# Performance work log

Measured on AMD Instinct MI355X. Metric: run time of the kernel, lower is better.

## Reference

```python
import jax, jax.numpy as jnp
import numpy as np

HIDDEN = 768

def setup_inputs() -> dict:
    key = jax.random.key(0)
    ks = jax.random.split(key, 7)
    x = jax.random.normal(ks[0], (4, 4096, HIDDEN), dtype=jnp.float32)
    s = 1.0 / np.sqrt(HIDDEN)
    Wq = jax.random.uniform(ks[1], (HIDDEN, HIDDEN), minval=-s, maxval=s, dtype=jnp.float32)
    Wk = jax.random.uniform(ks[2], (HIDDEN, HIDDEN), minval=-s, maxval=s, dtype=jnp.float32)
    Wv = jax.random.uniform(ks[3], (HIDDEN, HIDDEN), minval=-s, maxval=s, dtype=jnp.float32)
    bq = jax.random.uniform(ks[4], (HIDDEN,), minval=-s, maxval=s, dtype=jnp.float32)
    bk = jax.random.uniform(ks[5], (HIDDEN,), minval=-s, maxval=s, dtype=jnp.float32)
    bv = jax.random.uniform(ks[6], (HIDDEN,), minval=-s, maxval=s, dtype=jnp.float32)
    return {"x": x, "Wq": Wq, "bq": bq, "Wk": Wk, "bk": bk, "Wv": Wv, "bv": bv}

def reference(x, Wq, bq, Wk, bk, Wv, bv):
    # q,k,v: [b, s, d]
    q = jnp.einsum('bsd,de->bse', x, Wq.T) + bq
    k = jnp.einsum('bsd,de->bse', x, Wk.T) + bk
    v = jnp.einsum('bsd,de->bse', x, Wv.T) + bv
    scale = 1.0 / jnp.sqrt(jnp.asarray(x.shape[-1], dtype=x.dtype))
    scores = jnp.einsum('bqd,bkd->bqk', q, k) * scale  # [b, s, s]
    attn = jax.nn.softmax(scores, axis=-1)
    return jnp.einsum('bqk,bkd->bqd', attn, v)
```

## Files before the change

### kernel.cpp

```cpp
#include <hip/hip_runtime.h>
#include <stdint.h>

typedef unsigned short u16;
typedef __attribute__((ext_vector_type(8))) short    bf16x8;
typedef __attribute__((ext_vector_type(4))) float    f32x4;

__device__ __forceinline__ u16 f2bf(float f) {
    unsigned u = __float_as_uint(f);
    u = (u + 0x7fffu + ((u >> 16) & 1u)) >> 16;
    return (u16)u;
}

__device__ __forceinline__ void gload16(const u16* src, u16* dst) {
    __builtin_amdgcn_global_load_lds((const __attribute__((address_space(1))) void*)src,
                                     (__attribute__((address_space(3))) void*)dst,
                                     16, 0, 0);
}

template <int IMM>
__device__ __forceinline__ bf16x8 dsr128(uint32_t addr) {
    bf16x8 r;
    asm volatile("ds_read_b128 %0, %1 offset:%2" : "=v"(r) : "v"(addr), "i"(IMM));
    return r;
}

#define LA(ARR) ((uint32_t)(uintptr_t)(__attribute__((address_space(3))) void*)&(ARR)[0])

__global__ __launch_bounds__(256) void cast_all_kernel(const float* __restrict__ x,
                                                       const float* __restrict__ w0,
                                                       const float* __restrict__ w1,
                                                       const float* __restrict__ w2,
                                                       u16* __restrict__ xb,
                                                       u16* __restrict__ wb) {
    const int b = blockIdx.x;
    if (b < 12288) {
        int i = b * 256 + threadIdx.x;
        float4 f = ((const float4*)x)[i];
        ushort4 o;
        o.x = f2bf(f.x); o.y = f2bf(f.y); o.z = f2bf(f.z); o.w = f2bf(f.w);
        ((ushort4*)xb)[i] = o;
    } else {
        const int i2 = b - 12288;
        const int w  = i2 / 576;
        const int blk = i2 - w * 576;
        const float* src = (w == 0) ? w0 : (w == 1) ? w1 : w2;
        int i = blk * 256 + threadIdx.x;
        float4 f = ((const float4*)src)[i];
        ushort4 o;
        o.x = f2bf(f.x); o.y = f2bf(f.y); o.z = f2bf(f.z); o.w = f2bf(f.w);
        ((ushort4*)wb)[(size_t)w * 147456 + i] = o;
    }
}

__global__ __launch_bounds__(256) void transpose_bf16_kernel(const u16* __restrict__ V,
                                                             u16* __restrict__ Vt,
                                                             float* __restrict__ rsum) {
    __shared__ u16 tile[32][33];
    const int t = threadIdx.x;
    if (blockIdx.x == 0 && blockIdx.z == 0) {
        int idx = blockIdx.y * 256 + t;
        if (idx < 16384) rsum[idx] = 0.f;
    }
    const size_t z = blockIdx.z;
    const u16* Vb  = V  + z * (size_t)4096 * 2304;
    u16*       Vtb = Vt + z * (size_t)768 * 4096;
    const int c0 = blockIdx.x * 32;
    const int r0 = blockIdx.y * 32;
    const int lr = t >> 3;
    const int lc = (t & 7) * 4;
    ushort4 in = *(const ushort4*)&Vb[(size_t)(r0 + lr) * 2304 + c0 + lc];
    tile[lr][lc + 0] = in.x; tile[lr][lc + 1] = in.y;
    tile[lr][lc + 2] = in.z; tile[lr][lc + 3] = in.w;
    __syncthreads();
    ushort4 o;
    o.x = tile[lc + 0][lr]; o.y = tile[lc + 1][lr];
    o.z = tile[lc + 2][lr]; o.w = tile[lc + 3][lr];
    *(ushort4*)&Vtb[(size_t)(c0 + lr) * 4096 + r0 + lc] = o;
}

template <int EPI, int WN, int NBX, int GRP, int NGRID, int NBY, int MINW>
__global__ __launch_bounds__(256, MINW) void gemm_bt_kernel(
        const u16* __restrict__ A, const u16* __restrict__ B, void* __restrict__ Cv,
        const float* __restrict__ b0, const float* __restrict__ b1, const float* __restrict__ b2,
        float* __restrict__ rs, float s2, int K,
        int lda, int ldb, int ldc, long batchA, long batchB, long batchC) {
    __shared__ __align__(16) u16 As[128 * 64];
    __shared__ __align__(16) u16 Bs[32 * WN * 64];

    constexpr int SPX = NGRID / (8 * NBX);
    const int lin = blockIdx.x;
    const int c = lin & 7, p = lin >> 3;
    const int bxi = p % GRP;
    const int rest = p / GRP;
    const int s = rest % SPX;
    const int g = rest / SPX;
    const int bx = g * GRP + bxi;
    const int strip = c * SPX + s;
    const int by = strip % NBY;
    const int bz = strip / NBY;

    const int t = threadIdx.x;
    const long z = bz;
    const u16* Ab = A + z * batchA + (long)by * 128 * lda;
    const u16* Bb = B + z * batchB + (long)bx * (32 * WN) * ldb;

    const int lane = t & 63;
    const int wave = t >> 6;
    const int wm = wave >> 1, wn = wave & 1;
    const int quad = lane >> 4;
    const int frow = lane & 15;
    const int cc0 = quad ^ (frow & 7);

    f32x4 acc[4][WN];
#pragma unroll
    for (int i = 0; i < 4; i++)
#pragma unroll
        for (int j = 0; j < WN; j++)
#pragma unroll
            for (int e = 0; e < 4; e++) acc[i][j][e] = 0.f;

    int srow[WN], scol[WN];
#pragma unroll
    for (int j = 0; j < WN; j++) {
        const int d = t + j * 256;
        srow[j] = d >> 3;
        scol[j] = ((d & 7) ^ (srow[j] & 7)) * 8;
    }

    bf16x8 ra[4], rb[WN];
#pragma unroll
    for (int j = 0; j < 4; j++)
        ra[j] = *(const bf16x8*)(Ab + (long)srow[j] * lda + scol[j]);
#pragma unroll
    for (int j = 0; j < WN; j++)
        rb[j] = *(const bf16x8*)(Bb + (long)srow[j] * ldb + scol[j]);

    for (int kt = 0; kt < K; kt += 64) {
#pragma unroll
        for (int j = 0; j < 4; j++)
            *(bf16x8*)&As[(t + j * 256) * 8] = ra[j];
#pragma unroll
        for (int j = 0; j < WN; j++)
            *(bf16x8*)&Bs[(t + j * 256) * 8] = rb[j];
        __syncthreads();

        if (kt + 64 < K) {
            const int kn = kt + 64;
#pragma unroll
            for (int j = 0; j < 4; j++)
                ra[j] = *(const bf16x8*)(Ab + (long)srow[j] * lda + kn + scol[j]);
#pragma unroll
            for (int j = 0; j < WN; j++)
                rb[j] = *(const bf16x8*)(Bb + (long)srow[j] * ldb + kn + scol[j]);
        }

#pragma unroll
        for (int kk = 0; kk < 2; kk++) {
            const int cc = (cc0 ^ (kk * 4)) * 8;
            bf16x8 bfr[WN];
#pragma unroll
            for (int j = 0; j < WN; j++)
                bfr[j] = *(const bf16x8*)&Bs[(wn * WN * 16 + j * 16 + frow) * 64 + cc];
#pragma unroll
            for (int i = 0; i < 4; i++) {
                bf16x8 af = *(const bf16x8*)&As[(wm * 64 + i * 16 + frow) * 64 + cc];
#pragma unroll
                for (int j = 0; j < WN; j++)
                    acc[i][j] = __builtin_amdgcn_mfma_f32_16x16x32_bf16(af, bfr[j], acc[i][j], 0, 0, 0);
            }
        }
        __syncthreads();
    }

    const int m_base = by * 128 + wm * 64;
    const int n_base = bx * (32 * WN) + wn * (16 * WN);

    if (EPI == 0) {
        const int seg = n_base / 768;
        const float* bp = (seg == 0) ? b0 : (seg == 1) ? b1 : b2;
        u16* C = (u16*)Cv + z * batchC;
#pragma unroll
        for (int j = 0; j < WN; j++) {
            const int col = n_base + j * 16 + frow;
            const float bb = bp[col - seg * 768];
#pragma unroll
            for (int i = 0; i < 4; i++) {
                const int row0 = m_base + i * 16 + quad * 4;
#pragma unroll
                for (int r = 0; r < 4; r++)
                    C[(long)(row0 + r) * ldc + col] = f2bf(acc[i][j][r] + bb);
            }
        }
    } else if (EPI == 1) {
        u16* C = (u16*)Cv + z * batchC;
        float rowpart[4][4];
#pragma unroll
        for (int i = 0; i < 4; i++)
#pragma unroll
            for (int r = 0; r < 4; r++) rowpart[i][r] = 0.f;
#pragma unroll
        for (int i = 0; i < 4; i++) {
            const int row0 = m_base + i * 16 + quad * 4;
#pragma unroll
            for (int j = 0; j < WN; j++) {
                const int col = n_base + j * 16 + frow;
#pragma unroll
                for (int r = 0; r < 4; r++) {
                    float e = exp2f(acc[i][j][r] * s2);
                    C[(long)(row0 + r) * ldc + col] = f2bf(e);
                    rowpart[i][r] += e;
                }
            }
        }
#pragma unroll
        for (int i = 0; i < 4; i++)
#pragma unroll
            for (int r = 0; r < 4; r++) {
                float v = rowpart[i][r];
                v += __shfl_xor(v, 1); v += __shfl_xor(v, 2);
                v += __shfl_xor(v, 4); v += __shfl_xor(v, 8);
                if (frow == 0)
                    atomicAdd(&rs[z * 4096 + m_base + i * 16 + quad * 4 + r], v);
            }
    } else {
        float* C = (float*)Cv + z * batchC;
#pragma unroll
        for (int i = 0; i < 4; i++) {
            const int row0 = m_base + i * 16 + quad * 4;
            float inv[4];
#pragma unroll
            for (int r = 0; r < 4; r++) inv[r] = 1.0f / rs[z * 4096 + row0 + r];
#pragma unroll
            for (int j = 0; j < WN; j++) {
                const int col = n_base + j * 16 + frow;
#pragma unroll
                for (int r = 0; r < 4; r++)
                    C[(long)(row0 + r) * ldc + col] = acc[i][j][r] * inv[r];
            }
        }
    }
}

template <int NBX, int NBY, int GRP, int NGRID>
__global__ __launch_bounds__(512, 4) void gemm_tp_kernel(
        const u16* __restrict__ A, const u16* __restrict__ B, u16* __restrict__ C,
        float* __restrict__ rs, float s2, int K,
        int lda, int ldb, int ldc, long batchA, long batchB, long batchC) {
    __shared__ __align__(16) u16 As0[4096];
    __shared__ __align__(16) u16 As1[4096];
    __shared__ __align__(16) u16 Bs0[8192];
    __shared__ __align__(16) u16 Bs1[8192];

    constexpr int SPX = NGRID / (8 * NBX);
    const int lin = blockIdx.x;
    const int c = lin & 7, p = lin >> 3;
    const int bxi = p % GRP;
    const int rest = p / GRP;
    const int s = rest % SPX;
    const int g = rest / SPX;
    const int bx = g * GRP + bxi;
    const int strip = c * SPX + s;
    const int by = strip % NBY;
    const int bz = strip / NBY;

    const int t = threadIdx.x;
    const int lane = t & 63;
    const int wave = t >> 6;
    const int wm = wave >> 2, wn = wave & 3;
    const int quad = lane >> 4, frow = lane & 15;

    const u16* Ab = A + (long)bz * batchA + (long)by * 128 * lda;
    const u16* Bb = B + (long)bz * batchB + (long)bx * 256 * ldb;

    const int srow = ((t >> 3) << 1) | ((t >> 2) & 1);
    const int scol = ((t & 3) ^ ((t >> 3) & 3)) * 8;

    const uint32_t rdo2 = (uint32_t)(((frow >> 1) * 64
                        + ((frow & 1) * 4 + (quad ^ ((frow >> 1) & 3))) * 8) * 2);
    const uint32_t aof2 = (uint32_t)(wm * 2048 * 2) + rdo2;
    const uint32_t bof2 = (uint32_t)(wn * 2048 * 2) + rdo2;

    f32x4 acc[4][4];
#pragma unroll
    for (int i = 0; i < 4; i++)
#pragma unroll
        for (int j = 0; j < 4; j++)
#pragma unroll
            for (int e = 0; e < 4; e++) acc[i][j][e] = 0.f;

    auto SA = [&](u16* dst, int kofs) {
        gload16(Ab + (long)srow * lda + kofs + scol, dst + wave * 512);
    };
    auto SB = [&](u16* dst, int kofs) {
        gload16(Bb + (long)srow * ldb + kofs + scol, dst + wave * 512);
        gload16(Bb + (long)(srow + 128) * ldb + kofs + scol, dst + wave * 512 + 4096);
    };

    SA(As0, 0);  SB(Bs0, 0);
    SA(As1, 32); SB(Bs1, 32);

#define MFMA16(AF, BF)                                                           \
    __builtin_amdgcn_s_setprio(1);                                               \
    _Pragma("unroll")                                                            \
    for (int i = 0; i < 4; ++i)                                                  \
        _Pragma("unroll")                                                        \
        for (int j = 0; j < 4; ++j)                                              \
            acc[i][j] = __builtin_amdgcn_mfma_f32_16x16x32_bf16(                 \
                AF[i], BF[j], acc[i][j], 0, 0, 0);                               \
    __builtin_amdgcn_s_setprio(0);

    for (int kt = 0; kt < K; kt += 64) {
        const bool pre = (kt + 64 < K);
        bf16x8 af[4], bf[4];

        asm volatile("s_waitcnt vmcnt(3)" ::: "memory");
        __builtin_amdgcn_s_barrier();
        {
            const uint32_t aAd = LA(As0) + aof2;
            const uint32_t aBd = LA(Bs0) + bof2;
            af[0] = dsr128<0>(aAd);    af[1] = dsr128<1024>(aAd);
            af[2] = dsr128<2048>(aAd); af[3] = dsr128<3072>(aAd);
            bf[0] = dsr128<0>(aBd);    bf[1] = dsr128<1024>(aBd);
            bf[2] = dsr128<2048>(aBd); bf[3] = dsr128<3072>(aBd);
        }
        asm volatile("s_waitcnt lgkmcnt(0)" ::: "memory");
        __builtin_amdgcn_sched_barrier(0);
        __builtin_amdgcn_s_barrier();
        if (pre) { SA(As0, kt + 64); SB(Bs0, kt + 64); }
        __builtin_amdgcn_sched_barrier(0);
        MFMA16(af, bf)

        if (pre) asm volatile("s_waitcnt vmcnt(3)" ::: "memory");
        else     asm volatile("s_waitcnt vmcnt(0)" ::: "memory");
        __builtin_amdgcn_s_barrier();
        {
            const uint32_t aAd = LA(As1) + aof2;
            const uint32_t aBd = LA(Bs1) + bof2;
            af[0] = dsr128<0>(aAd);    af[1] = dsr128<1024>(aAd);
            af[2] = dsr128<2048>(aAd); af[3] = dsr128<3072>(aAd);
            bf[0] = dsr128<0>(aBd);    bf[1] = dsr128<1024>(aBd);
            bf[2] = dsr128<2048>(aBd); bf[3] = dsr128<3072>(aBd);
        }
        asm volatile("s_waitcnt lgkmcnt(0)" ::: "memory");
        __builtin_amdgcn_sched_barrier(0);
        __builtin_amdgcn_s_barrier();
        if (pre) { SA(As1, kt + 96); SB(Bs1, kt + 96); }
        __builtin_amdgcn_sched_barrier(0);
        MFMA16(af, bf)
    }
#undef MFMA16

    const int m_base = by * 128 + wm * 64;
    const int n_base = bx * 256 + wn * 64;
    const long z = bz;
    u16* Cb = C + z * batchC;
#pragma unroll
    for (int i = 0; i < 4; ++i) {
        const int row0 = m_base + i * 16 + quad * 4;
        float rp[4] = {0.f, 0.f, 0.f, 0.f};
#pragma unroll
        for (int j = 0; j < 4; ++j) {
            const int col = n_base + j * 16 + frow;
#pragma unroll
            for (int r = 0; r < 4; ++r) {
                float e = exp2f(acc[i][j][r] * s2);
                Cb[(long)(row0 + r) * ldc + col] = f2bf(e);
                rp[r] += e;
            }
        }
#pragma unroll
        for (int r = 0; r < 4; ++r) {
            float v = rp[r];
            v += __shfl_xor(v, 1); v += __shfl_xor(v, 2);
            v += __shfl_xor(v, 4); v += __shfl_xor(v, 8);
            if (frow == 0) atomicAdd(&rs[z * 4096 + row0 + r], v);
        }
    }
}

extern "C" void kernel_launch(void* const* d_in, const int* in_sizes, int n_in,
                              void* d_out, int out_size, void* d_ws, size_t ws_size,
                              hipStream_t stream) {
    const float* x  = (const float*)d_in[0];
    const float* Wq = (const float*)d_in[1];
    const float* bq = (const float*)d_in[2];
    const float* Wk = (const float*)d_in[3];
    const float* bk = (const float*)d_in[4];
    const float* Wv = (const float*)d_in[5];
    const float* bv = (const float*)d_in[6];
    float* out = (float*)d_out;

    uint8_t* ws = (uint8_t*)d_ws;
    u16*   xb   = (u16*)(ws + 0);
    u16*   Vt   = (u16*)(ws + 0);
    u16*   QKV  = (u16*)(ws + 25165824);
    u16*   E    = (u16*)(ws + 100663296);
    u16*   Wqkv = (u16*)(ws + 234881024);
    float* rsum = (float*)(ws + 234881024);

    cast_all_kernel<<<14016, 256, 0, stream>>>(x, Wq, Wk, Wv, xb, Wqkv);

    gemm_bt_kernel<0, 4, 18, 6, 2304, 128, 3><<<2304, 256, 0, stream>>>(
        xb, Wqkv, QKV, bq, bk, bv, nullptr, 0.f, 768, 768, 768, 2304, 0, 0, 0);

    transpose_bf16_kernel<<<dim3(24, 128, 4), 256, 0, stream>>>(QKV + 1536, Vt, rsum);

    gemm_tp_kernel<16, 32, 4, 2048><<<2048, 512, 0, stream>>>(
        QKV, QKV + 768, E, rsum, 0.05205954822032348f, 768,
        2304, 2304, 4096, (long)4096 * 2304, (long)4096 * 2304, (long)4096 * 4096);

    gemm_bt_kernel<2, 4, 6, 6, 768, 32, 3><<<768, 256, 0, stream>>>(
        E, Vt, out, nullptr, nullptr, nullptr, rsum, 0.f,
        4096, 4096, 4096, 768, (long)4096 * 4096, (long)768 * 4096, (long)4096 * 768);
}
```

Baseline: 414.3 us.

## Swap QK^T to generic GEMM and add dedicated 128-thread PV kernel

The QK^T exp/rowsum stage now runs on the generic gemm_bt_kernel in a mode 1 configuration instead of the specialised 512-thread tile kernel. The former tp kernel is repurposed into a 128-thread, 2-wave-per-SIMD PV kernel with 128x128 tiles, each wave computing 128x64 with 8x4 MFMA accumulators, normalising by the row sums on output. The aim is better tile shapes and reuse for each of the two attention GEMMs. In exchange the PV kernel carries heavy register pressure and low occupancy, and correctness depends on gemm_bt mode 1 computing exp and rowsum as the old kernel did.

```diff
diff --git a/kernel.cpp b/kernel.cpp
--- a/kernel.cpp
+++ b/kernel.cpp
@@ -242,14 +242,14 @@
 }
 
 template <int NBX, int NBY, int GRP, int NGRID>
-__global__ __launch_bounds__(512, 4) void gemm_tp_kernel(
-        const u16* __restrict__ A, const u16* __restrict__ B, u16* __restrict__ C,
-        float* __restrict__ rs, float s2, int K,
+__global__ __launch_bounds__(128, 2) void gemm_pv_kernel(
+        const u16* __restrict__ A, const u16* __restrict__ B, float* __restrict__ C,
+        const float* __restrict__ rs, int K,
         int lda, int ldb, int ldc, long batchA, long batchB, long batchC) {
     __shared__ __align__(16) u16 As0[4096];
     __shared__ __align__(16) u16 As1[4096];
-    __shared__ __align__(16) u16 Bs0[8192];
-    __shared__ __align__(16) u16 Bs1[8192];
+    __shared__ __align__(16) u16 Bs0[4096];
+    __shared__ __align__(16) u16 Bs1[4096];
 
     constexpr int SPX = NGRID / (8 * NBX);
     const int lin = blockIdx.x;
@@ -265,115 +265,110 @@
 
     const int t = threadIdx.x;
     const int lane = t & 63;
-    const int wave = t >> 6;
-    const int wm = wave >> 2, wn = wave & 3;
+    const int wn = t >> 6;
     const int quad = lane >> 4, frow = lane & 15;
 
     const u16* Ab = A + (long)bz * batchA + (long)by * 128 * lda;
-    const u16* Bb = B + (long)bz * batchB + (long)bx * 256 * ldb;
-
-    const int srow = ((t >> 3) << 1) | ((t >> 2) & 1);
-    const int scol = ((t & 3) ^ ((t >> 3) & 3)) * 8;
+    const u16* Bb = B + (long)bz * batchB + (long)bx * 128 * ldb;
 
     const uint32_t rdo2 = (uint32_t)(((frow >> 1) * 64
                         + ((frow & 1) * 4 + (quad ^ ((frow >> 1) & 3))) * 8) * 2);
-    const uint32_t aof2 = (uint32_t)(wm * 2048 * 2) + rdo2;
-    const uint32_t bof2 = (uint32_t)(wn * 2048 * 2) + rdo2;
-
-    f32x4 acc[4][4];
-#pragma unroll
-    for (int i = 0; i < 4; i++)
+    const uint32_t bofs = (uint32_t)(wn * 4096);
+
+    f32x4 acc[8][4];
+#pragma unroll
+    for (int i = 0; i < 8; i++)
 #pragma unroll
         for (int j = 0; j < 4; j++)
 #pragma unroll
             for (int e = 0; e < 4; e++) acc[i][j][e] = 0.f;
 
-    auto SA = [&](u16* dst, int kofs) {
-        gload16(Ab + (long)srow * lda + kofs + scol, dst + wave * 512);
+    const int wbase = (t & 64) * 8;
+    auto SS = [&](u16* dst, const u16* gb, int ld_, int kofs) {
+#pragma unroll
+        for (int q = 0; q < 4; ++q) {
+            const int dd = q * 128 + t;
+            const int sr = ((dd >> 3) << 1) | ((dd >> 2) & 1);
+            const int sc = ((dd & 3) ^ ((dd >> 3) & 3)) * 8;
+            gload16(gb + (long)sr * ld_ + kofs + sc, dst + q * 1024 + wbase);
+        }
     };
-    auto SB = [&](u16* dst, int kofs) {
-        gload16(Bb + (long)srow * ldb + kofs + scol, dst + wave * 512);
-        gload16(Bb + (long)(srow + 128) * ldb + kofs + scol, dst + wave * 512 + 4096);
-    };
-
-    SA(As0, 0);  SB(Bs0, 0);
-    SA(As1, 32); SB(Bs1, 32);
-
-#define MFMA16(AF, BF)                                                           \
+
+#define MFMA32(AF, BF)                                                           \
     __builtin_amdgcn_s_setprio(1);                                               \
     _Pragma("unroll")                                                            \
-    for (int i = 0; i < 4; ++i)                                                  \
+    for (int i = 0; i < 8; ++i)                                                  \
         _Pragma("unroll")                                                        \
         for (int j = 0; j < 4; ++j)                                              \
             acc[i][j] = __builtin_amdgcn_mfma_f32_16x16x32_bf16(                 \
                 AF[i], BF[j], acc[i][j], 0, 0, 0);                               \
     __builtin_amdgcn_s_setprio(0);
 
+    SS(As0, Ab, lda, 0);  SS(Bs0, Bb, ldb, 0);
+    SS(As1, Ab, lda, 32); SS(Bs1, Bb, ldb, 32);
+
     for (int kt = 0; kt < K; kt += 64) {
         const bool pre = (kt + 64 < K);
-        bf16x8 af[4], bf[4];
-
-        asm volatile("s_waitcnt vmcnt(3)" ::: "memory");
+        bf16x8 af[8], bf[4];
+
+        asm volatile("s_waitcnt vmcnt(8)" ::: "memory");
         __builtin_amdgcn_s_barrier();
         {
-            const uint32_t aAd = LA(As0) + aof2;
-            const uint32_t aBd = LA(Bs0) + bof2;
-            af[0] = dsr128<0>(aAd);    af[1] = dsr128<1024>(aAd);
-            af[2] = dsr128<2048>(aAd); af[3] = dsr128<3072>(aAd);
-            bf[0] = dsr128<0>(aBd);    bf[1] = dsr128<1024>(aBd);
-            bf[2] = dsr128<2048>(aBd); bf[3] = dsr128<3072>(aBd);
+            const uint32_t aA = LA(As0) + rdo2;
+            const uint32_t aB = LA(Bs0) + bofs + rdo2;
+            af[0] = dsr128<0>(aA);    af[1] = dsr128<1024>(aA);
+            af[2] = dsr128<2048>(aA); af[3] = dsr128<3072>(aA);
+            af[4] = dsr128<4096>(aA); af[5] = dsr128<5120>(aA);
+            af[6] = dsr128<6144>(aA); af[7] = dsr128<7168>(aA);
+            bf[0] = dsr128<0>(aB);    bf[1] = dsr128<1024>(aB);
+            bf[2] = dsr128<2048>(aB); bf[3] = dsr128<3072>(aB);
         }
         asm volatile("s_waitcnt lgkmcnt(0)" ::: "memory");
         __builtin_amdgcn_sched_barrier(0);
         __builtin_amdgcn_s_barrier();
-        if (pre) { SA(As0, kt + 64); SB(Bs0, kt + 64); }
+        if (pre) { SS(As0, Ab, lda, kt + 64); SS(Bs0, Bb, ldb, kt + 64); }
         __builtin_amdgcn_sched_barrier(0);
-        MFMA16(af, bf)
-
-        if (pre) asm volatile("s_waitcnt vmcnt(3)" ::: "memory");
+        MFMA32(af, bf)
+
+        if (pre) asm volatile("s_waitcnt vmcnt(8)" ::: "memory");
         else     asm volatile("s_waitcnt vmcnt(0)" ::: "memory");
         __builtin_amdgcn_s_barrier();
         {
-            const uint32_t aAd = LA(As1) + aof2;
-            const uint32_t aBd = LA(Bs1) + bof2;
-            af[0] = dsr128<0>(aAd);    af[1] = dsr128<1024>(aAd);
-            af[2] = dsr128<2048>(aAd); af[3] = dsr128<3072>(aAd);
-            bf[0] = dsr128<0>(aBd);    bf[1] = dsr128<1024>(aBd);
-            bf[2] = dsr128<2048>(aBd); bf[3] = dsr128<3072>(aBd);
+            const uint32_t aA = LA(As1) + rdo2;
+            const uint32_t aB = LA(Bs1) + bofs + rdo2;
+            af[0] = dsr128<0>(aA);    af[1] = dsr128<1024>(aA);
+            af[2] = dsr128<2048>(aA); af[3] = dsr128<3072>(aA);
+            af[4] = dsr128<4096>(aA); af[5] = dsr128<5120>(aA);
+            af[6] = dsr128<6144>(aA); af[7] = dsr128<7168>(aA);
+            bf[0] = dsr128<0>(aB);    bf[1] = dsr128<1024>(aB);
+            bf[2] = dsr128<2048>(aB); bf[3] = dsr128<3072>(aB);
         }
         asm volatile("s_waitcnt lgkmcnt(0)" ::: "memory");
         __builtin_amdgcn_sched_barrier(0);
         __builtin_amdgcn_s_barrier();
-        if (pre) { SA(As1, kt + 96); SB(Bs1, kt + 96); }
+        if (pre) { SS(As1, Ab, lda, kt + 96); SS(Bs1, Bb, ldb, kt + 96); }
         __builtin_amdgcn_sched_barrier(0);
-        MFMA16(af, bf)
-    }
-#undef MFMA16
-
-    const int m_base = by * 128 + wm * 64;
-    const int n_base = bx * 256 + wn * 64;
+        MFMA32(af, bf)
+    }
+#undef MFMA32
+
+    const int m_base = by * 128;
+    const int n_base = bx * 128 + wn * 64;
     const long z = bz;
-    u16* Cb = C + z * batchC;
-#pragma unroll
-    for (int i = 0; i < 4; ++i) {
+    float* Cb = C + z * batchC;
+    const float* rz = rs + z * 4096;
+#pragma unroll
+    for (int i = 0; i < 8; ++i) {
         const int row0 = m_base + i * 16 + quad * 4;
-        float rp[4] = {0.f, 0.f, 0.f, 0.f};
+        float inv[4];
+#pragma unroll
+        for (int r = 0; r < 4; ++r) inv[r] = 1.0f / rz[row0 + r];
 #pragma unroll
         for (int j = 0; j < 4; ++j) {
             const int col = n_base + j * 16 + frow;
 #pragma unroll
-            for (int r = 0; r < 4; ++r) {
-                float e = exp2f(acc[i][j][r] * s2);
-                Cb[(long)(row0 + r) * ldc + col] = f2bf(e);
-                rp[r] += e;
-            }
-        }
-#pragma unroll
-        for (int r = 0; r < 4; ++r) {
-            float v = rp[r];
-            v += __shfl_xor(v, 1); v += __shfl_xor(v, 2);
-            v += __shfl_xor(v, 4); v += __shfl_xor(v, 8);
-            if (frow == 0) atomicAdd(&rs[z * 4096 + row0 + r], v);
+            for (int r = 0; r < 4; ++r)
+                Cb[(long)(row0 + r) * ldc + col] = acc[i][j][r] * inv[r];
         }
     }
 }
@@ -405,11 +400,11 @@
 
     transpose_bf16_kernel<<<dim3(24, 128, 4), 256, 0, stream>>>(QKV + 1536, Vt, rsum);
 
-    gemm_tp_kernel<16, 32, 4, 2048><<<2048, 512, 0, stream>>>(
-        QKV, QKV + 768, E, rsum, 0.05205954822032348f, 768,
-        2304, 2304, 4096, (long)4096 * 2304, (long)4096 * 2304, (long)4096 * 4096);
-
-    gemm_bt_kernel<2, 4, 6, 6, 768, 32, 3><<<768, 256, 0, stream>>>(
-        E, Vt, out, nullptr, nullptr, nullptr, rsum, 0.f,
-        4096, 4096, 4096, 768, (long)4096 * 4096, (long)768 * 4096, (long)4096 * 768);
-}
+    gemm_bt_kernel<1, 8, 16, 4, 2048, 32, 2><<<2048, 256, 0, stream>>>(
+        QKV, QKV + 768, E, nullptr, nullptr, nullptr, rsum, 0.05205954822032348f,
+        768, 2304, 2304, 4096, (long)4096 * 2304, (long)4096 * 2304, (long)4096 * 4096);
+
+    gemm_pv_kernel<6, 32, 6, 768><<<768, 128, 0, stream>>>(
+        E, Vt, out, rsum, 4096,
+        4096, 4096, 768, (long)4096 * 4096, (long)768 * 4096, (long)4096 * 768);
+}
```

Result: slower. 428.2 us (+3.3%).
